# Performance work log

Measured on AMD Instinct MI355X. Metric: run time of the kernel, lower is better.

## Reference

```python
import jax, jax.numpy as jnp
import numpy as np

IN_FEATURES = 4096
OUT_FEATURES = 11008
QMIN, QMAX = -128, 127


def setup_inputs() -> dict:
    key = jax.random.key(0)
    k_in, k_w, k_s, k_z, k_b = jax.random.split(key, 5)
    inp = jax.random.normal(k_in, (4, 2048, IN_FEATURES), dtype=jnp.float32)
    # int8 quantized weight in [qmin, qmax]
    weight_quantized = jax.random.randint(
        k_w, (OUT_FEATURES, IN_FEATURES), QMIN, QMAX + 1, dtype=jnp.int32
    ).astype(jnp.int8)
    # per-output-row scale / zero point (shape [out, 1] as in the module)
    weight_scale = jax.random.uniform(k_s, (OUT_FEATURES, 1), dtype=jnp.float32,
                                      minval=0.005, maxval=0.02)
    weight_zero_point = jax.random.uniform(k_z, (OUT_FEATURES, 1), dtype=jnp.float32,
                                           minval=-4.0, maxval=4.0)
    bias = jax.random.normal(k_b, (OUT_FEATURES,), dtype=jnp.float32) * 0.01
    return {
        "input": inp,
        "weight_quantized": weight_quantized,
        "weight_scale": weight_scale,
        "weight_zero_point": weight_zero_point,
        "bias": bias,
    }


def reference(input, weight_quantized, weight_scale, weight_zero_point, bias):
    # Dequantize: per-row affine, W_f32[o, i] = (q[o, i] - zp[o]) * scale[o]
    weight_float = (weight_quantized.astype(jnp.float32) - weight_zero_point) * weight_scale
    # F.linear: y = x @ W^T + b   -> [B, S, out]
    out = jnp.einsum("bsi,oi->bso", input, weight_float) + bias
    return out
```

## Files before the change

kernel.cpp:

```cpp
#include <hip/hip_runtime.h>

#define K_DIM 4096
#define N_DIM 11008
#define M_DIM 8192
#define NT 64

typedef _Float16 f16;
typedef f16 f16x4 __attribute__((ext_vector_type(4)));
typedef f16 f16x8 __attribute__((ext_vector_type(8)));
typedef float f32x4 __attribute__((ext_vector_type(4)));

typedef __attribute__((address_space(1))) unsigned int gu32;
typedef __attribute__((address_space(3))) unsigned int lu32;

__device__ __forceinline__ void g2l16(const void* gp, void* lp) {
    __builtin_amdgcn_global_load_lds((gu32*)gp, (lu32*)lp, 16, 0, 0);
}

__global__ __launch_bounds__(256) void convw_kernel(const int* __restrict__ Wq,
                                                    f16* __restrict__ Wh) {
    const size_t n4 = (size_t)N_DIM * K_DIM / 4;
    const size_t stride = (size_t)gridDim.x * 256;
    const int4* src = (const int4*)Wq;
    f16x4* dst = (f16x4*)Wh;
    for (size_t i = (size_t)blockIdx.x * 256 + threadIdx.x; i < n4; i += stride) {
        int4 a = src[i];
        f16x4 o = {(f16)a.x, (f16)a.y, (f16)a.z, (f16)a.w};
        dst[i] = o;
    }
}

__global__ __launch_bounds__(256) void convx_kernel(const float* __restrict__ X,
                                                    f16* __restrict__ Xh,
                                                    float* __restrict__ rs) {
    const int row = blockIdx.x;
    const int t = threadIdx.x;
    const float4* xr = (const float4*)(X + (size_t)row * K_DIM);
    f16x4* xo = (f16x4*)(Xh + (size_t)row * K_DIM);
    float s = 0.f;
#pragma unroll
    for (int j = 0; j < 4; ++j) {
        float4 v = xr[t + 256 * j];
        f16x4 h = {(f16)v.x, (f16)v.y, (f16)v.z, (f16)v.w};
        xo[t + 256 * j] = h;
        s += (float)h[0] + (float)h[1] + (float)h[2] + (float)h[3];
    }
#pragma unroll
    for (int off = 32; off > 0; off >>= 1) s += __shfl_down(s, off);
    __shared__ float part[4];
    if ((t & 63) == 0) part[t >> 6] = s;
    __syncthreads();
    if (t == 0) rs[row] = part[0] + part[1] + part[2] + part[3];
}

__global__ __launch_bounds__(512, 2)
void qlin_gemm(const f16* __restrict__ Xh, const f16* __restrict__ Wh,
               const float* __restrict__ scale, const float* __restrict__ zp,
               const float* __restrict__ bias, const float* __restrict__ rowsum,
               float* __restrict__ out) {
    extern __shared__ __align__(16) char smem[];

    const int t = threadIdx.x;
    const int l = t & 63;
    const int w = t >> 6;
    const int wm = w >> 2;
    const int wn = w & 3;
    const int q = l >> 4;
    const int ln = l & 15;

    const int m0 = blockIdx.x * 256;
    const int n0 = blockIdx.y * 256;

    const int srow = t >> 3;
    const int sslot = (t & 7) ^ (srow & 7);
    const char* xbase = (const char*)Xh + ((size_t)(m0 + srow) << 13) + (sslot << 4);
    const char* wbase = (const char*)Wh + ((size_t)(n0 + srow) << 13) + (sslot << 4);
    char* ldst = smem + t * 16;

#define STG_A(p, c, T) g2l16(xbase + ((size_t)(c) << 19) + ((size_t)(T) << 7), ldst + (p)*65536 + (c)*8192)
#define STG_B(p, c, T) g2l16(wbase + ((size_t)(c) << 19) + ((size_t)(T) << 7), ldst + (p)*65536 + 32768 + (c)*8192)
#define SB __builtin_amdgcn_sched_barrier(0)
#define BAR __builtin_amdgcn_s_barrier()
#define LGKM0 asm volatile("s_waitcnt lgkmcnt(0)" ::: "memory")

    const int xs = ln & 7;
    int offA[2], offB[2];
    offA[0] = (wm * 128 + ln) * 128 + ((q ^ xs) << 4);
    offA[1] = (wm * 128 + ln) * 128 + (((q + 4) ^ xs) << 4);
    offB[0] = 32768 + (wn * 64 + ln) * 128 + ((q ^ xs) << 4);
    offB[1] = 32768 + (wn * 64 + ln) * 128 + (((q + 4) ^ xs) << 4);

    f32x4 acc[8][4] = {};
    f16x8 aR[4][2], bR[4][2];

    STG_A(0, 0, 0); STG_A(0, 2, 0); STG_B(0, 0, 0); STG_B(0, 1, 0);
    STG_A(0, 1, 0); STG_A(0, 3, 0); STG_B(0, 2, 0); STG_B(0, 3, 0);
    STG_A(1, 0, 1); STG_A(1, 2, 1); STG_B(1, 0, 1); STG_B(1, 1, 1);
    STG_A(1, 1, 1); STG_A(1, 3, 1);
    asm volatile("s_waitcnt vmcnt(6)" ::: "memory");
    BAR;

#define TILE(T, CUR)                                                                               \
    do {                                                                                           \
                       \
        _Pragma("unroll") for (int kk = 0; kk < 2; ++kk) {                                         \
            _Pragma("unroll") for (int i = 0; i < 4; ++i)                                          \
                aR[i][kk] = *(const f16x8*)(smem + (CUR)*65536 + offA[kk] + i * 2048);             \
            _Pragma("unroll") for (int j = 0; j < 2; ++j)                                          \
                bR[j][kk] = *(const f16x8*)(smem + (CUR)*65536 + offB[kk] + j * 2048);             \
        }                                                                                          \
        if ((T) + 1 < NT) { STG_B(((CUR) ^ 1), 2, (T) + 1); STG_B(((CUR) ^ 1), 3, (T) + 1); }      \
        SB; BAR; LGKM0; SB;                                                                        \
        __builtin_amdgcn_s_setprio(1);                                                             \
        _Pragma("unroll") for (int kk = 0; kk < 2; ++kk)                                           \
            _Pragma("unroll") for (int i = 0; i < 4; ++i)                                          \
                _Pragma("unroll") for (int j = 0; j < 2; ++j)                                      \
                    acc[i][j] = __builtin_amdgcn_mfma_f32_16x16x32_f16(aR[i][kk], bR[j][kk],       \
                                                                       acc[i][j], 0, 0, 0);        \
        __builtin_amdgcn_s_setprio(0);                                                             \
        SB; BAR; SB;                                                                               \
                                  \
        _Pragma("unroll") for (int kk = 0; kk < 2; ++kk) {                                         \
            _Pragma("unroll") for (int j = 0; j < 2; ++j)                                          \
                bR[2 + j][kk] = *(const f16x8*)(smem + (CUR)*65536 + offB[kk] + (2 + j) * 2048);   \
        }                                                                                          \
        if ((T) + 2 < NT) { STG_A((CUR), 0, (T) + 2); STG_A((CUR), 2, (T) + 2); }                  \
        SB; BAR; LGKM0; SB;                                                                        \
        __builtin_amdgcn_s_setprio(1);                                                             \
        _Pragma("unroll") for (int kk = 0; kk < 2; ++kk)                                           \
            _Pragma("unroll") for (int i = 0; i < 4; ++i)                                          \
                _Pragma("unroll") for (int j = 0; j < 2; ++j)                                      \
                    acc[i][2 + j] = __builtin_amdgcn_mfma_f32_16x16x32_f16(aR[i][kk],              \
                                        bR[2 + j][kk], acc[i][2 + j], 0, 0, 0);                    \
        __builtin_amdgcn_s_setprio(0);                                                             \
        SB; BAR; SB;                                                                               \
                                  \
        _Pragma("unroll") for (int kk = 0; kk < 2; ++kk) {                                         \
            _Pragma("unroll") for (int i = 0; i < 4; ++i)                                          \
                aR[i][kk] = *(const f16x8*)(smem + (CUR)*65536 + offA[kk] + (4 + i) * 2048);       \
        }                                                                                          \
        if ((T) + 2 < NT) { STG_B((CUR), 0, (T) + 2); STG_B((CUR), 1, (T) + 2); }                  \
        SB; BAR; LGKM0; SB;                                                                        \
        __builtin_amdgcn_s_setprio(1);                                                             \
        _Pragma("unroll") for (int kk = 0; kk < 2; ++kk)                                           \
            _Pragma("unroll") for (int i = 0; i < 4; ++i)                                          \
                _Pragma("unroll") for (int j = 0; j < 2; ++j)                                      \
                    acc[4 + i][2 + j] = __builtin_amdgcn_mfma_f32_16x16x32_f16(aR[i][kk],          \
                                            bR[2 + j][kk], acc[4 + i][2 + j], 0, 0, 0);            \
        __builtin_amdgcn_s_setprio(0);                                                             \
        SB; BAR; SB;                                                                               \
                              \
        if ((T) + 2 < NT) {                                                                        \
            STG_A((CUR), 1, (T) + 2); STG_A((CUR), 3, (T) + 2);                                    \
            asm volatile("s_waitcnt vmcnt(6)" ::: "memory");                                       \
        } else {                                                                                   \
            asm volatile("s_waitcnt vmcnt(0)" ::: "memory");                                       \
        }                                                                                          \
        SB; BAR; SB;                                                                               \
        __builtin_amdgcn_s_setprio(1);                                                             \
        _Pragma("unroll") for (int kk = 0; kk < 2; ++kk)                                           \
            _Pragma("unroll") for (int i = 0; i < 4; ++i)                                          \
                _Pragma("unroll") for (int j = 0; j < 2; ++j)                                      \
                    acc[4 + i][j] = __builtin_amdgcn_mfma_f32_16x16x32_f16(aR[i][kk], bR[j][kk],   \
                                        acc[4 + i][j], 0, 0, 0);                                   \
        __builtin_amdgcn_s_setprio(0);                                                             \
        SB; BAR; SB;                                                                               \
    } while (0)

#pragma unroll 1
    for (int Tp = 0; Tp < NT / 2; ++Tp) {
        TILE(2 * Tp, 0);
        TILE(2 * Tp + 1, 1);
    }
#undef TILE
#undef STG_A
#undef STG_B

    float sc[4], zv[4], bv[4];
    int ncol[4];
#pragma unroll
    for (int j = 0; j < 4; ++j) {
        const int n = n0 + wn * 64 + j * 16 + ln;
        ncol[j] = n;
        sc[j] = scale[n];
        zv[j] = zp[n];
        bv[j] = bias[n];
    }
#pragma unroll
    for (int i = 0; i < 8; ++i) {
#pragma unroll
        for (int r = 0; r < 4; ++r) {
            const int m = m0 + wm * 128 + i * 16 + q * 4 + r;
            const float rsm = rowsum[m];
            const size_t rowoff = (size_t)m * N_DIM;
#pragma unroll
            for (int j = 0; j < 4; ++j) {
                out[rowoff + ncol[j]] = sc[j] * (acc[i][j][r] - zv[j] * rsm) + bv[j];
            }
        }
    }
}

extern "C" void kernel_launch(void* const* d_in, const int* in_sizes, int n_in,
                              void* d_out, int out_size, void* d_ws, size_t ws_size,
                              hipStream_t stream) {
    const float* X     = (const float*)d_in[0];
    const int*   Wq    = (const int*)d_in[1];
    const float* scale = (const float*)d_in[2];
    const float* zp    = (const float*)d_in[3];
    const float* bias  = (const float*)d_in[4];
    float* out = (float*)d_out;

    f16* Wh = (f16*)d_ws;
    f16* Xh = (f16*)((char*)d_ws + (size_t)N_DIM * K_DIM * 2);
    float* rowsum = (float*)((char*)d_ws + (size_t)N_DIM * K_DIM * 2 + (size_t)M_DIM * K_DIM * 2);

    static bool attr_done = false;
    if (!attr_done) {
        (void)hipFuncSetAttribute((const void*)qlin_gemm,
                                  hipFuncAttributeMaxDynamicSharedMemorySize, 131072);
        attr_done = true;
    }

    convw_kernel<<<4096, 256, 0, stream>>>(Wq, Wh);
    convx_kernel<<<M_DIM, 256, 0, stream>>>(X, Xh, rowsum);

    dim3 grid(M_DIM / 256, N_DIM / 256);
    qlin_gemm<<<grid, 512, 131072, stream>>>(Xh, Wh, scale, zp, bias, rowsum, out);
}
```

Before: 1.160 ms.

## Software-pipeline LDS reads with MFMA blocks and peel final tiles

Restructures the main loop so LDS fragment reads for the next sub-block are issued alongside the current MFMA block, instead of waiting behind a barrier before each compute phase. B fragments are split into separate b01/b23 register sets so both halves stay live across phases, and the next tile's A-low/B01 reads are prefetched at the end of each body. The last two tiles are peeled out of the loop, which removes the per-iteration bounds checks on global-to-LDS staging. This adds register pressure and barrier-ordering complexity in exchange for hiding LDS latency.

```diff
diff --git a/kernel.cpp b/kernel.cpp
--- a/kernel.cpp
+++ b/kernel.cpp
@@ -82,6 +82,7 @@
 #define SB __builtin_amdgcn_sched_barrier(0)
 #define BAR __builtin_amdgcn_s_barrier()
 #define LGKM0 asm volatile("s_waitcnt lgkmcnt(0)" ::: "memory")
+#define VMC6 asm volatile("s_waitcnt vmcnt(6)" ::: "memory")
 
     const int xs = ln & 7;
     int offA[2], offB[2];
@@ -91,90 +92,83 @@
     offB[1] = 32768 + (wn * 64 + ln) * 128 + (((q + 4) ^ xs) << 4);
 
     f32x4 acc[8][4] = {};
-    f16x8 aR[4][2], bR[4][2];
+    f16x8 aR[4][2], b01[2][2], b23[2][2];
+
+#define RD_ALO(P)                                                              \
+    _Pragma("unroll") for (int kk = 0; kk < 2; ++kk)                           \
+    _Pragma("unroll") for (int i = 0; i < 4; ++i)                              \
+        aR[i][kk] = *(const f16x8*)(smem + (P)*65536 + offA[kk] + i * 2048)
+#define RD_AHI(P)                                                              \
+    _Pragma("unroll") for (int kk = 0; kk < 2; ++kk)                           \
+    _Pragma("unroll") for (int i = 0; i < 4; ++i)                              \
+        aR[i][kk] = *(const f16x8*)(smem + (P)*65536 + offA[kk] + (4 + i) * 2048)
+#define RD_B01(P)                                                              \
+    _Pragma("unroll") for (int kk = 0; kk < 2; ++kk)                           \
+    _Pragma("unroll") for (int j = 0; j < 2; ++j)                              \
+        b01[j][kk] = *(const f16x8*)(smem + (P)*65536 + offB[kk] + j * 2048)
+#define RD_B23(P)                                                              \
+    _Pragma("unroll") for (int kk = 0; kk < 2; ++kk)                           \
+    _Pragma("unroll") for (int j = 0; j < 2; ++j)                              \
+        b23[j][kk] = *(const f16x8*)(smem + (P)*65536 + offB[kk] + (2 + j) * 2048)
+#define MFMA_BLK(I0, J0, BSET)                                                 \
+    _Pragma("unroll") for (int kk = 0; kk < 2; ++kk)                           \
+    _Pragma("unroll") for (int i = 0; i < 4; ++i)                              \
+    _Pragma("unroll") for (int j = 0; j < 2; ++j)                              \
+        acc[(I0) + i][(J0) + j] = __builtin_amdgcn_mfma_f32_16x16x32_f16(      \
+            aR[i][kk], BSET[j][kk], acc[(I0) + i][(J0) + j], 0, 0, 0)
 
     STG_A(0, 0, 0); STG_A(0, 2, 0); STG_B(0, 0, 0); STG_B(0, 1, 0);
     STG_A(0, 1, 0); STG_A(0, 3, 0); STG_B(0, 2, 0); STG_B(0, 3, 0);
     STG_A(1, 0, 1); STG_A(1, 2, 1); STG_B(1, 0, 1); STG_B(1, 1, 1);
     STG_A(1, 1, 1); STG_A(1, 3, 1);
-    asm volatile("s_waitcnt vmcnt(6)" ::: "memory");
-    BAR;
-
-#define TILE(T, CUR)                                                                               \
-    do {                                                                                           \
-                       \
-        _Pragma("unroll") for (int kk = 0; kk < 2; ++kk) {                                         \
-            _Pragma("unroll") for (int i = 0; i < 4; ++i)                                          \
-                aR[i][kk] = *(const f16x8*)(smem + (CUR)*65536 + offA[kk] + i * 2048);             \
-            _Pragma("unroll") for (int j = 0; j < 2; ++j)                                          \
-                bR[j][kk] = *(const f16x8*)(smem + (CUR)*65536 + offB[kk] + j * 2048);             \
-        }                                                                                          \
-        if ((T) + 1 < NT) { STG_B(((CUR) ^ 1), 2, (T) + 1); STG_B(((CUR) ^ 1), 3, (T) + 1); }      \
-        SB; BAR; LGKM0; SB;                                                                        \
-        __builtin_amdgcn_s_setprio(1);                                                             \
-        _Pragma("unroll") for (int kk = 0; kk < 2; ++kk)                                           \
-            _Pragma("unroll") for (int i = 0; i < 4; ++i)                                          \
-                _Pragma("unroll") for (int j = 0; j < 2; ++j)                                      \
-                    acc[i][j] = __builtin_amdgcn_mfma_f32_16x16x32_f16(aR[i][kk], bR[j][kk],       \
-                                                                       acc[i][j], 0, 0, 0);        \
-        __builtin_amdgcn_s_setprio(0);                                                             \
-        SB; BAR; SB;                                                                               \
-                                  \
-        _Pragma("unroll") for (int kk = 0; kk < 2; ++kk) {                                         \
-            _Pragma("unroll") for (int j = 0; j < 2; ++j)                                          \
-                bR[2 + j][kk] = *(const f16x8*)(smem + (CUR)*65536 + offB[kk] + (2 + j) * 2048);   \
-        }                                                                                          \
-        if ((T) + 2 < NT) { STG_A((CUR), 0, (T) + 2); STG_A((CUR), 2, (T) + 2); }                  \
-        SB; BAR; LGKM0; SB;                                                                        \
-        __builtin_amdgcn_s_setprio(1);                                                             \
-        _Pragma("unroll") for (int kk = 0; kk < 2; ++kk)                                           \
-            _Pragma("unroll") for (int i = 0; i < 4; ++i)                                          \
-                _Pragma("unroll") for (int j = 0; j < 2; ++j)                                      \
-                    acc[i][2 + j] = __builtin_amdgcn_mfma_f32_16x16x32_f16(aR[i][kk],              \
-                                        bR[2 + j][kk], acc[i][2 + j], 0, 0, 0);                    \
-        __builtin_amdgcn_s_setprio(0);                                                             \
-        SB; BAR; SB;                                                                               \
-                                  \
-        _Pragma("unroll") for (int kk = 0; kk < 2; ++kk) {                                         \
-            _Pragma("unroll") for (int i = 0; i < 4; ++i)                                          \
-                aR[i][kk] = *(const f16x8*)(smem + (CUR)*65536 + offA[kk] + (4 + i) * 2048);       \
-        }                                                                                          \
-        if ((T) + 2 < NT) { STG_B((CUR), 0, (T) + 2); STG_B((CUR), 1, (T) + 2); }                  \
-        SB; BAR; LGKM0; SB;                                                                        \
-        __builtin_amdgcn_s_setprio(1);                                                             \
-        _Pragma("unroll") for (int kk = 0; kk < 2; ++kk)                                           \
-            _Pragma("unroll") for (int i = 0; i < 4; ++i)                                          \
-                _Pragma("unroll") for (int j = 0; j < 2; ++j)                                      \
-                    acc[4 + i][2 + j] = __builtin_amdgcn_mfma_f32_16x16x32_f16(aR[i][kk],          \
-                                            bR[2 + j][kk], acc[4 + i][2 + j], 0, 0, 0);            \
-        __builtin_amdgcn_s_setprio(0);                                                             \
-        SB; BAR; SB;                                                                               \
-                              \
-        if ((T) + 2 < NT) {                                                                        \
-            STG_A((CUR), 1, (T) + 2); STG_A((CUR), 3, (T) + 2);                                    \
-            asm volatile("s_waitcnt vmcnt(6)" ::: "memory");                                       \
-        } else {                                                                                   \
-            asm volatile("s_waitcnt vmcnt(0)" ::: "memory");                                       \
-        }                                                                                          \
-        SB; BAR; SB;                                                                               \
-        __builtin_amdgcn_s_setprio(1);                                                             \
-        _Pragma("unroll") for (int kk = 0; kk < 2; ++kk)                                           \
-            _Pragma("unroll") for (int i = 0; i < 4; ++i)                                          \
-                _Pragma("unroll") for (int j = 0; j < 2; ++j)                                      \
-                    acc[4 + i][j] = __builtin_amdgcn_mfma_f32_16x16x32_f16(aR[i][kk], bR[j][kk],   \
-                                        acc[4 + i][j], 0, 0, 0);                                   \
-        __builtin_amdgcn_s_setprio(0);                                                             \
-        SB; BAR; SB;                                                                               \
-    } while (0)
+    VMC6; SB; BAR; SB;
+    RD_ALO(0); RD_B01(0);
+    STG_B(1, 2, 1); STG_B(1, 3, 1);
+    LGKM0; SB; BAR; SB;
+
+#define BODY(T, CUR)                                                           \
+                          \
+    RD_B23(CUR);                                                               \
+    MFMA_BLK(0, 0, b01);                                                       \
+    STG_A(CUR, 0, (T) + 2); STG_A(CUR, 2, (T) + 2);                            \
+    LGKM0; SB; BAR; SB;                                                        \
+              \
+    MFMA_BLK(0, 2, b23);                                                       \
+    RD_AHI(CUR);                                                               \
+    STG_B(CUR, 0, (T) + 2); STG_B(CUR, 1, (T) + 2);                            \
+    LGKM0; SB; BAR; SB;                                                        \
+                 \
+    MFMA_BLK(4, 2, b23);                                                       \
+    STG_A(CUR, 1, (T) + 2); STG_A(CUR, 3, (T) + 2);                            \
+    VMC6; SB; BAR; SB;                                                         \
+         \
+    MFMA_BLK(4, 0, b01);                                                       \
+    RD_ALO((CUR) ^ 1); RD_B01((CUR) ^ 1);                                      \
+    STG_B(CUR, 2, (T) + 2); STG_B(CUR, 3, (T) + 2);                            \
+    LGKM0; SB; BAR; SB;
 
 #pragma unroll 1
-    for (int Tp = 0; Tp < NT / 2; ++Tp) {
-        TILE(2 * Tp, 0);
-        TILE(2 * Tp + 1, 1);
-    }
-#undef TILE
-#undef STG_A
-#undef STG_B
+    for (int Tp = 0; Tp < 31; ++Tp) {
+        const int Tb = 2 * Tp;
+        BODY(Tb, 0);
+        BODY(Tb + 1, 1);
+    }
+#undef BODY
+
+    RD_B23(0);
+    MFMA_BLK(0, 0, b01);
+    MFMA_BLK(0, 2, b23);
+    RD_AHI(0);
+    MFMA_BLK(4, 2, b23);
+    asm volatile("s_waitcnt vmcnt(0)" ::: "memory");
+    SB; BAR; SB;
+    MFMA_BLK(4, 0, b01);
+    RD_ALO(1); RD_B01(1); RD_B23(1);
+    MFMA_BLK(0, 0, b01);
+    MFMA_BLK(0, 2, b23);
+    RD_AHI(1);
+    MFMA_BLK(4, 2, b23);
+    MFMA_BLK(4, 0, b01);
 
     float sc[4], zv[4], bv[4];
     int ncol[4];
```

New measurement: 1.103 ms. 1.05x faster.
